# Kernel tuning notes

Measured on AMD Instinct MI355X. Metric: run time of the kernel, lower is better.

The kernel has to match this reference:

```python
import jax, jax.numpy as jnp
import numpy as np

EPS = 1e-5

def conv(x, w, b, stride, pad):
    y = jax.lax.conv_general_dilated(x, w, (stride, stride), [(pad, pad), (pad, pad)],
                                     dimension_numbers=('NCHW', 'OIHW', 'NCHW'))
    return y + b[None, :, None, None]

def inorm(x):
    # InstanceNorm2d, affine=False, eps=1e-5, biased variance over H,W
    m = x.mean(axis=(2, 3), keepdims=True)
    v = ((x - m) ** 2).mean(axis=(2, 3), keepdims=True)
    return (x - m) * jax.lax.rsqrt(v + EPS)

def setup_inputs() -> dict:
    key = jax.random.key(0)
    ks = jax.random.split(key, 24)
    B = 64
    x = jax.random.normal(ks[0], (B, 5, 256, 192), dtype=jnp.float32)
    chans = [(5, 8), (8, 16), (16, 32), (32, 64), (64, 128), (128, 256)]
    params = {'x': x}
    for i, (ci, co) in enumerate(chans):
        fan = ci * 16
        params[f'w{i}'] = jax.random.normal(ks[1 + 2 * i], (co, ci, 4, 4), jnp.float32) / np.sqrt(fan)
        params[f'b{i}'] = jnp.zeros((co,), jnp.float32)
    for i in (6, 7):
        params[f'w{i}'] = jax.random.normal(ks[1 + 2 * i], (256, 256, 3, 3), jnp.float32) / np.sqrt(256 * 9)
        params[f'b{i}'] = jnp.zeros((256,), jnp.float32)
    params['fc1_w'] = jax.random.normal(ks[20], (128, 512), jnp.float32) / np.sqrt(512)
    params['fc1_b'] = jnp.zeros((128,), jnp.float32)
    # fc2: weight zeroed at init in original; use small random for a nontrivial baseline
    params['fc2_w'] = jax.random.normal(ks[21], (50, 128), jnp.float32) * 0.01
    lin = np.linspace(-0.9, 0.9, 5, dtype=np.float32)
    yy, xx = np.meshgrid(lin, lin, indexing='ij')
    tcp = np.stack([xx.ravel(), yy.ravel()], axis=1)  # [25,2]
    params['fc2_b'] = jnp.asarray(np.arctanh(tcp).reshape(-1))  # [50]
    return params

def reference(x, w0, b0, w1, b1, w2, b2, w3, b3, w4, b4, w5, b5, w6, b6, w7, b7,
              fc1_w, fc1_b, fc2_w, fc2_b):
    B = x.shape[0]
    # block 0: conv -> relu -> instance_norm
    h = inorm(jax.nn.relu(conv(x, w0, b0, 2, 1)))
    # blocks 1..5: conv -> instance_norm -> relu, stride 2
    for w, b in ((w1, b1), (w2, b2), (w3, b3), (w4, b4), (w5, b5)):
        h = jax.nn.relu(inorm(conv(h, w, b, 2, 1)))
    # two 3x3 stride-1 blocks
    for w, b in ((w6, b6), (w7, b7)):
        h = jax.nn.relu(inorm(conv(h, w, b, 1, 1)))
    # maxpool 2x2 stride 2
    h = jax.lax.reduce_window(h, -jnp.inf, jax.lax.max, (1, 1, 2, 2), (1, 1, 2, 2), 'VALID')
    h = h.reshape(B, -1)  # [B,512]
    h = jax.nn.relu(h @ fc1_w.T + fc1_b)
    # F.dropout in eval mode = identity (reference is deterministic)
    pts = jnp.tanh(h @ fc2_w.T + fc2_b)  # [B,50]
    coor = pts.reshape(B, -1, 2)          # [B,25,2]
    grid = coor.reshape(B, 5, 5, 2)       # [B, row j, col i, (x,y)]

    # get_row: squared diffs along i, then abs second difference; stack order (j outer, i inner)
    d_row = (grid[:, :, 1:] - grid[:, :, :-1]) ** 2            # [B,5,4,2]
    row = jnp.abs(d_row[:, :, 1:] - d_row[:, :, :-1]).reshape(B, 15, 2)
    # get_col: same along j; stack order (i outer, j inner)
    gT = jnp.swapaxes(grid, 1, 2)                              # [B, i, j, 2]
    d_col = (gT[:, :, 1:] - gT[:, :, :-1]) ** 2
    col = jnp.abs(d_col[:, :, 1:] - d_col[:, :, :-1]).reshape(B, 15, 2)

    # grad_row / grad_col: curvature cross-product terms, BATCH ELEMENT 0 ONLY (as in original)
    def curv(g):  # g: [5,5,2], triplets along axis 1
        p0, p1, p2 = g[:, :-2], g[:, 1:-1], g[:, 2:]
        x0, y0 = p0[..., 0], p0[..., 1]
        x1, y1 = p1[..., 0], p1[..., 1]
        x2, y2 = p2[..., 0], p2[..., 1]
        return jnp.abs((y1 - y0) * (x1 - x2) - (y1 - y2) * (x1 - x0))  # [5,3]

    g0 = grid[0]
    rg_loss = jnp.maximum(curv(g0).sum(), 0.02)
    cg_loss = jnp.maximum(curv(jnp.swapaxes(g0, 0, 1)).sum(), 0.02)

    rx_loss = jnp.maximum(0.08, row[:, :, 0]).mean()
    ry_loss = jnp.maximum(0.08, row[:, :, 1]).mean()
    cx_loss = jnp.maximum(0.08, col[:, :, 0]).mean()
    cy_loss = jnp.maximum(0.08, col[:, :, 1]).mean()
    return (coor, rx_loss, ry_loss, cx_loss, cy_loss, rg_loss, cg_loss)
```

## Files before the change

### kernel.cpp

```cpp
#include <hip/hip_runtime.h>
#include <hip/hip_bf16.h>
#include <math.h>

#define EPS 1e-5f

template<int CIN, int COUT, int H, int W, int TPB>
__global__ __launch_bounds__(TPB) void conv42V(const float* __restrict__ in,
                                               const float* __restrict__ w,
                                               const float* __restrict__ bias,
                                               float* __restrict__ out, int relu)
{
    constexpr int OH  = H / 2, OW = W / 2;
    constexpr int NPX = OH * OW;
    constexpr int PXB = (NPX / 2) / TPB;
    constexpr int NCG = COUT / 8;

    __shared__ float sW[CIN * 8 * 16];
    __shared__ float sB[8];

    int t   = threadIdx.x;
    int bx  = blockIdx.x;
    int pxb = bx % PXB;
    int cg  = (bx / PXB) % NCG;
    int n   = bx / (PXB * NCG);
// ... 135 lines not shown

__global__ __launch_bounds__(256) void inorm_wave_T768(const float* __restrict__ src,
                                                       float* __restrict__ dst_t)
{
    int gid  = blockIdx.x * blockDim.x + threadIdx.x;
    int wv   = gid >> 6;
    int lane = gid & 63;
    int n = wv >> 5;
    int c = wv & 31;
    const float* p = src + (size_t)wv * 768;
    float tv[12];
    float s1 = 0.f, s2 = 0.f;
#pragma unroll
    for (int k = 0; k < 12; ++k) {
        float v = p[lane + k * 64];
        tv[k] = v;
        s1 += v; s2 += v * v;
    }
    for (int m = 32; m >= 1; m >>= 1) {
        s1 += __shfl_xor(s1, m);
        s2 += __shfl_xor(s2, m);
    }
    float mean = s1 * (1.f / 768.f);
    float var  = s2 * (1.f / 768.f) - mean * mean;
    float r = rsqrtf(var + EPS);
#pragma unroll
    for (int k = 0; k < 12; ++k) {
        int i = lane + k * 64;
        float y = fmaxf((tv[k] - mean) * r, 0.f);
        dst_t[((size_t)c * 768 + i) * 64 + n] = y;
    }
}

__global__ __launch_bounds__(256) void conv_l3t(const float* __restrict__ in_t,
                                                const float* __restrict__ w,
                                                float* __restrict__ pbuf)
{
    int t    = threadIdx.x;
    int lane = t & 63;
    int gw   = __builtin_amdgcn_readfirstlane(blockIdx.x * 4 + (t >> 6));
    int cog  = gw & 31;
    int cic  = (gw >> 5) & 3;
    int oh   = gw >> 7;
    int cc   = cic * 8;
    int co0  = cog * 2;
    int ih0  = 2 * oh - 1;

    float acc[2][12];
#pragma unroll
    for (int j = 0; j < 2; ++j)
#pragma unroll
        for (int p = 0; p < 12; ++p) acc[j][p] = 0.f;

    const float* wb = w + ((size_t)co0 * 32 + cc) * 16;

#pragma unroll 1
    for (int ci = 0; ci < 8; ++ci) {
        const float* pl = in_t + (size_t)(cc + ci) * 768 * 64 + lane;
        float wr[2][16];
#pragma unroll
        for (int k = 0; k < 16; ++k) {
            wr[0][k] = wb[(0 * 32 + ci) * 16 + k];
            wr[1][k] = wb[(1 * 32 + ci) * 16 + k];
        }
#pragma unroll
        for (int kh = 0; kh < 4; ++kh) {
            int ih = ih0 + kh;
            float p[26];
            p[0] = 0.f; p[25] = 0.f;
            if ((unsigned)ih < 32u) {
#pragma unroll
                for (int c = 0; c < 24; ++c)
                    p[c + 1] = pl[(size_t)(ih * 24 + c) * 64];
            } else {
#pragma unroll
                for (int c = 0; c < 24; ++c) p[c + 1] = 0.f;
            }
#pragma unroll
            for (int ow = 0; ow < 12; ++ow) {
#pragma unroll
                for (int kw = 0; kw < 4; ++kw) {
                    float pv = p[2 * ow + kw];
                    acc[0][ow] = fmaf(pv, wr[0][kh * 4 + kw], acc[0][ow]);
                    acc[1][ow] = fmaf(pv, wr[1][kh * 4 + kw], acc[1][ow]);
                }
            }
        }
    }

    float* pb = pbuf + ((size_t)cic * 4096 + (size_t)lane * 64 + co0) * 192 + oh * 12;
#pragma unroll
    for (int j = 0; j < 2; ++j) {
        float4* o4 = (float4*)(pb + (size_t)j * 192);
        o4[0] = make_float4(acc[j][0], acc[j][1], acc[j][2],  acc[j][3]);
        o4[1] = make_float4(acc[j][4], acc[j][5], acc[j][6],  acc[j][7]);
        o4[2] = make_float4(acc[j][8], acc[j][9], acc[j][10], acc[j][11]);
    }
}

__global__ __launch_bounds__(256) void reduce_norm_l3T(const float* __restrict__ pbuf,
                                                       float* __restrict__ dst_t)
{
    int gid  = blockIdx.x * blockDim.x + threadIdx.x;
    int wv   = gid >> 6;
    int lane = gid & 63;
    int n  = wv >> 6;
    int co = wv & 63;
    float tv[3];
#pragma unroll
    for (int k = 0; k < 3; ++k) {
        int i = lane + k * 64;
        float sum = 0.f;
#pragma unroll
        for (int s = 0; s < 4; ++s)
            sum += pbuf[((size_t)s * 4096 + wv) * 192 + i];
        tv[k] = sum;
    }
    float s1 = tv[0] + tv[1] + tv[2];
    float s2 = tv[0]*tv[0] + tv[1]*tv[1] + tv[2]*tv[2];
    for (int m = 32; m >= 1; m >>= 1) {
        s1 += __shfl_xor(s1, m);
        s2 += __shfl_xor(s2, m);
    }
    float mean = s1 * (1.f / 192.f);
    float var  = s2 * (1.f / 192.f) - mean * mean;
    float r = rsqrtf(var + EPS);
#pragma unroll
    for (int k = 0; k < 3; ++k) {
        int i = lane + k * 64;
        float y = fmaxf((tv[k] - mean) * r, 0.f);
        dst_t[((size_t)co * 192 + i) * 64 + n] = y;
    }
}

template<int TPB, int VPT>
__global__ void inorm_blockv(float* __restrict__ data, int relu)
{
    const int HW = TPB * VPT * 4;
    float4* p = (float4*)(data + (size_t)blockIdx.x * HW);
    float4 v[VPT];
    float s = 0.f, q = 0.f;
#pragma unroll
    for (int k = 0; k < VPT; ++k) {
        v[k] = p[threadIdx.x + k * TPB];
        s += v[k].x + v[k].y + v[k].z + v[k].w;
        q += v[k].x*v[k].x + v[k].y*v[k].y + v[k].z*v[k].z + v[k].w*v[k].w;
    }
    for (int m2 = 32; m2 >= 1; m2 >>= 1) {
        s += __shfl_xor(s, m2);
        q += __shfl_xor(q, m2);
    }
    __shared__ float ss[TPB / 64], sq[TPB / 64], sm[2];
    int wave = threadIdx.x >> 6, lane = threadIdx.x & 63;
    if (lane == 0) { ss[wave] = s; sq[wave] = q; }
    __syncthreads();
    if (threadIdx.x == 0) {
        float a = 0.f, b2 = 0.f;
#pragma unroll
        for (int k = 0; k < TPB / 64; ++k) { a += ss[k]; b2 += sq[k]; }
        float mm = a / (float)HW;
        float vv = b2 / (float)HW - mm * mm;
        sm[0] = mm; sm[1] = rsqrtf(vv + EPS);
    }
    __syncthreads();
    float m = sm[0], r = sm[1];
#pragma unroll
    for (int k = 0; k < VPT; ++k) {
        float4 y;
        y.x = (v[k].x - m) * r; y.y = (v[k].y - m) * r;
        y.z = (v[k].z - m) * r; y.w = (v[k].w - m) * r;
        if (relu) {
            y.x = fmaxf(y.x, 0.f); y.y = fmaxf(y.y, 0.f);
            y.z = fmaxf(y.z, 0.f); y.w = fmaxf(y.w, 0.f);
        }
        p[threadIdx.x + k * TPB] = y;
    }
}

__global__ __launch_bounds__(256) void conv_l4(const float* __restrict__ in_t,
                                               const float* __restrict__ w,
                                               float* __restrict__ pbuf)
{
    int t    = threadIdx.x;
    int lane = t & 63;
    int gw   = __builtin_amdgcn_readfirstlane(blockIdx.x * 4 + (t >> 6));
    int cog  = gw & 63;
    int cic  = (gw >> 6) & 7;
    int half = gw >> 9;
    int cc   = cic * 8;
    int co0  = cog * 2;
    int oh0  = half * 4;

    float acc[2][24];
#pragma unroll
    for (int j = 0; j < 2; ++j)
#pragma unroll
        for (int p = 0; p < 24; ++p) acc[j][p] = 0.f;

    const float* wp = w + ((size_t)co0 * 64 + cc) * 16;

#pragma unroll 1
    for (int ci = 0; ci < 8; ++ci) {
        const float* pl = in_t + (size_t)(cc + ci) * 192 * 64 + lane;
        float wr[2][16];
#pragma unroll
        for (int k = 0; k < 16; ++k) {
            wr[0][k] = wp[(0 * 64 + ci) * 16 + k];
            wr[1][k] = wp[(1 * 64 + ci) * 16 + k];
        }
#pragma unroll
        for (int kh = 0; kh < 4; ++kh) {
            float p[4][12];
#pragma unroll
            for (int o = 0; o < 4; ++o) {
                int ih = 2 * (oh0 + o) - 1 + kh;
                if ((unsigned)ih < 16u) {
#pragma unroll
                    for (int c = 0; c < 12; ++c)
                        p[o][c] = pl[(size_t)(ih * 12 + c) * 64];
                } else {
#pragma unroll
                    for (int c = 0; c < 12; ++c) p[o][c] = 0.f;
                }
            }
#pragma unroll
            for (int o = 0; o < 4; ++o)
#pragma unroll
                for (int ow = 0; ow < 6; ++ow) {
#pragma unroll
                    for (int kw = 0; kw < 4; ++kw) {
                        int iw = 2 * ow - 1 + kw;
                        if (iw < 0 || iw >= 12) continue;
                        float pv = p[o][iw];
                        acc[0][o * 6 + ow] = fmaf(pv, wr[0][kh * 4 + kw], acc[0][o * 6 + ow]);
                        acc[1][o * 6 + ow] = fmaf(pv, wr[1][kh * 4 + kw], acc[1][o * 6 + ow]);
                    }
                }
        }
    }

    float* pb = pbuf + ((size_t)(cic * 64 + lane) * 128 + co0) * 48 + oh0 * 6;
#pragma unroll
    for (int j = 0; j < 2; ++j) {
        float4* o4 = (float4*)(pb + j * 48);
#pragma unroll
        for (int q = 0; q < 6; ++q)
            o4[q] = make_float4(acc[j][q * 4 + 0], acc[j][q * 4 + 1],
                                acc[j][q * 4 + 2], acc[j][q * 4 + 3]);
    }
}

__global__ __launch_bounds__(256) void reduce_norm48(const float* __restrict__ pbuf,
                                                     float* __restrict__ out)
{
    int g  = blockIdx.x * blockDim.x + threadIdx.x;
    int co = g & 127;
    int n  = g >> 7;
    float s[48];
#pragma unroll
    for (int p = 0; p < 48; ++p) s[p] = 0.f;
#pragma unroll 1
    for (int c = 0; c < 8; ++c) {
        const float4* p4 = (const float4*)(pbuf + ((size_t)(c * 64 + n) * 128 + co) * 48);
#pragma unroll
        for (int q = 0; q < 12; ++q) {
            float4 a = p4[q];
            s[q * 4 + 0] += a.x; s[q * 4 + 1] += a.y;
            s[q * 4 + 2] += a.z; s[q * 4 + 3] += a.w;
        }
    }
    float m = 0.f;
#pragma unroll
    for (int p = 0; p < 48; ++p) m += s[p];
    m *= (1.f / 48.f);
    float q = 0.f;
#pragma unroll
    for (int p = 0; p < 48; ++p) { float d = s[p] - m; q += d * d; }
    q *= (1.f / 48.f);
    float r = rsqrtf(q + EPS);
    float4* o4 = (float4*)(out + ((size_t)n * 128 + co) * 48);
#pragma unroll
    for (int qq = 0; qq < 12; ++qq) {
        float4 v;
        v.x = fmaxf((s[qq * 4 + 0] - m) * r, 0.f);
        v.y = fmaxf((s[qq * 4 + 1] - m) * r, 0.f);
        v.z = fmaxf((s[qq * 4 + 2] - m) * r, 0.f);
        v.w = fmaxf((s[qq * 4 + 3] - m) * r, 0.f);
        o4[qq] = v;
    }
}

__global__ __launch_bounds__(256) void conv_l67(const float* __restrict__ in,
                                                const float* __restrict__ w,
                                                float* __restrict__ pbuf)
{
    int t    = threadIdx.x;
    int gw   = __builtin_amdgcn_readfirstlane(blockIdx.x * 4 + (t >> 6));
    int lane = t & 63;
    int cic  = gw >> 6;
    int cog  = gw & 63;
    int cc   = cic * 16;
    int co0  = cog * 4;

    float acc[4][12];
#pragma unroll
    for (int j = 0; j < 4; ++j)
#pragma unroll
        for (int p = 0; p < 12; ++p) acc[j][p] = 0.f;

    const float* ip = in + ((size_t)lane * 256 + cc) * 12;
    const float* wp = w + ((size_t)co0 * 256 + cc) * 9;

#pragma unroll 2
    for (int ci = 0; ci < 16; ++ci) {
        float p[12];
        const float4* p4 = (const float4*)(ip + ci * 12);
        float4 a0 = p4[0], a1 = p4[1], a2 = p4[2];
        p[0] = a0.x; p[1] = a0.y; p[2]  = a0.z; p[3]  = a0.w;
        p[4] = a1.x; p[5] = a1.y; p[6]  = a1.z; p[7]  = a1.w;
        p[8] = a2.x; p[9] = a2.y; p[10] = a2.z; p[11] = a2.w;
#pragma unroll
        for (int j = 0; j < 4; ++j) {
            const float* wj = wp + ((size_t)j * 256 + ci) * 9;
            float wr[9];
#pragma unroll
            for (int k = 0; k < 9; ++k) wr[k] = wj[k];
#pragma unroll
            for (int oh = 0; oh < 4; ++oh)
#pragma unroll
                for (int ow = 0; ow < 3; ++ow)
#pragma unroll
                    for (int kh = 0; kh < 3; ++kh) {
                        int ih = oh - 1 + kh;
                        if (ih < 0 || ih >= 4) continue;
#pragma unroll
                        for (int kw = 0; kw < 3; ++kw) {
                            int iw = ow - 1 + kw;
                            if (iw < 0 || iw >= 3) continue;
                            acc[j][oh * 3 + ow] =
                                fmaf(p[ih * 3 + iw], wr[kh * 3 + kw], acc[j][oh * 3 + ow]);
                        }
                    }
        }
    }

    float* pb = pbuf + ((size_t)(cic * 64 + lane) * 256 + co0) * 12;
#pragma unroll
    for (int j = 0; j < 4; ++j) {
        float4* o4 = (float4*)(pb + j * 12);
        o4[0] = make_float4(acc[j][0], acc[j][1], acc[j][2],  acc[j][3]);
        o4[1] = make_float4(acc[j][4], acc[j][5], acc[j][6],  acc[j][7]);
        o4[2] = make_float4(acc[j][8], acc[j][9], acc[j][10], acc[j][11]);
    }
}

__global__ __launch_bounds__(256) void conv_l5(const float* __restrict__ in,
                                               const float* __restrict__ w,
                                               float* __restrict__ pbuf)
{
    int t    = threadIdx.x;
    int gw   = __builtin_amdgcn_readfirstlane(blockIdx.x * 4 + (t >> 6));
    int lane = t & 63;
    int cic  = gw >> 6;
    int cog  = gw & 63;
    int cc   = cic * 8;
    int co0  = cog * 4;

    float acc[4][12];
#pragma unroll
    for (int j = 0; j < 4; ++j)
#pragma unroll
        for (int p = 0; p < 12; ++p) acc[j][p] = 0.f;

    const float* ip = in + ((size_t)lane * 128 + cc) * 48;
    const float* wp = w + ((size_t)co0 * 128 + cc) * 16;

#pragma unroll 1
    for (int ci = 0; ci < 8; ++ci) {
        float p[48];
        const float4* p4 = (const float4*)(ip + ci * 48);
#pragma unroll
        for (int q = 0; q < 12; ++q) {
            float4 a = p4[q];
            p[q * 4 + 0] = a.x; p[q * 4 + 1] = a.y; p[q * 4 + 2] = a.z; p[q * 4 + 3] = a.w;
        }
#pragma unroll
        for (int j = 0; j < 4; ++j) {
            const float* wj = wp + ((size_t)j * 128 + ci) * 16;
            float wr[16];
#pragma unroll
            for (int k = 0; k < 16; ++k) wr[k] = wj[k];
#pragma unroll
            for (int oh = 0; oh < 4; ++oh)
#pragma unroll
                for (int ow = 0; ow < 3; ++ow) {
                    int ih0 = 2 * oh - 1, iw0 = 2 * ow - 1;
#pragma unroll
                    for (int kh = 0; kh < 4; ++kh) {
                        int ih = ih0 + kh;
                        if (ih < 0 || ih >= 8) continue;
#pragma unroll
                        for (int kw = 0; kw < 4; ++kw) {
                            int iw = iw0 + kw;
                            if (iw < 0 || iw >= 6) continue;
                            acc[j][oh * 3 + ow] =
                                fmaf(p[ih * 6 + iw], wr[kh * 4 + kw], acc[j][oh * 3 + ow]);
                        }
                    }
                }
        }
    }

    float* pb = pbuf + ((size_t)(cic * 64 + lane) * 256 + co0) * 12;
#pragma unroll
    for (int j = 0; j < 4; ++j) {
        float4* o4 = (float4*)(pb + j * 12);
        o4[0] = make_float4(acc[j][0], acc[j][1], acc[j][2],  acc[j][3]);
        o4[1] = make_float4(acc[j][4], acc[j][5], acc[j][6],  acc[j][7]);
        o4[2] = make_float4(acc[j][8], acc[j][9], acc[j][10], acc[j][11]);
    }
}

__global__ __launch_bounds__(256) void reduce_norm12(const float* __restrict__ pbuf,
                                                     float* __restrict__ out)
{
    int g  = blockIdx.x * blockDim.x + threadIdx.x;
    int co = g & 255;
    int n  = g >> 8;
    float s[12];
#pragma unroll
    for (int p = 0; p < 12; ++p) s[p] = 0.f;
#pragma unroll 1
    for (int c = 0; c < 16; ++c) {
        const float4* p4 = (const float4*)(pbuf + ((size_t)(c * 64 + n) * 256 + co) * 12);
        float4 a = p4[0], b = p4[1], d = p4[2];
        s[0] += a.x; s[1] += a.y; s[2]  += a.z; s[3]  += a.w;
        s[4] += b.x; s[5] += b.y; s[6]  += b.z; s[7]  += b.w;
        s[8] += d.x; s[9] += d.y; s[10] += d.z; s[11] += d.w;
    }
    float m = 0.f;
#pragma unroll
    for (int p = 0; p < 12; ++p) m += s[p];
    m *= (1.f / 12.f);
    float q = 0.f;
#pragma unroll
    for (int p = 0; p < 12; ++p) { float d = s[p] - m; q += d * d; }
    q *= (1.f / 12.f);
    float r = rsqrtf(q + EPS);
    float* op = out + ((size_t)n * 256 + co) * 12;
    float4* o4 = (float4*)op;
    float y[12];
#pragma unroll
    for (int p = 0; p < 12; ++p) y[p] = fmaxf((s[p] - m) * r, 0.f);
    o4[0] = make_float4(y[0], y[1], y[2],  y[3]);
    o4[1] = make_float4(y[4], y[5], y[6],  y[7]);
    o4[2] = make_float4(y[8], y[9], y[10], y[11]);
}

__global__ void pool_kernel(const float* __restrict__ in, float* __restrict__ out)
{
    int idx = blockIdx.x * blockDim.x + threadIdx.x;
    if (idx >= 64 * 512) return;
    int f = idx & 511;
    int n = idx >> 9;
    int c = f >> 1;
    int h = f & 1;
    const float* p = in + (((size_t)n * 256 + c) * 4 + h * 2) * 3;
    out[idx] = fmaxf(fmaxf(p[0], p[1]), fmaxf(p[3], p[4]));
}

__global__ void fc1_kernel(const float* __restrict__ in, const float* __restrict__ w,
                           const float* __restrict__ b, float* __restrict__ out)
{
    int idx = blockIdx.x * blockDim.x + threadIdx.x;
    if (idx >= 64 * 128) return;
    int j = idx & 127;
    int n = idx >> 7;
    const float* x  = in + n * 512;
    const float* wr = w + j * 512;
    float acc = b[j];
    for (int f = 0; f < 512; ++f) acc = fmaf(x[f], wr[f], acc);
    out[idx] = fmaxf(acc, 0.f);
}

__global__ void fc2_kernel(const float* __restrict__ in, const float* __restrict__ w,
                           const float* __restrict__ b, float* __restrict__ out)
{
    int idx = blockIdx.x * blockDim.x + threadIdx.x;
    if (idx >= 64 * 50) return;
    int k = idx % 50;
    int n = idx / 50;
    const float* x  = in + n * 128;
    const float* wr = w + k * 128;
    float acc = b[k];
    for (int f = 0; f < 128; ++f) acc = fmaf(x[f], wr[f], acc);
    out[idx] = tanhf(acc);
}

__global__ void loss_kernel(const float* __restrict__ pts, float* __restrict__ out)
{
    __shared__ float acc[4][64];
    int n = threadIdx.x;
    float rx = 0.f, ry = 0.f, cx = 0.f, cy = 0.f;
    {
        const float* g = pts + n * 50;
        for (int r = 0; r < 5; ++r)
            for (int j = 0; j < 3; ++j)
                for (int d = 0; d < 2; ++d) {
                    float a0 = g[(r * 5 + j) * 2 + d];
                    float a1 = g[(r * 5 + j + 1) * 2 + d];
                    float a2 = g[(r * 5 + j + 2) * 2 + d];
                    float d0 = (a1 - a0) * (a1 - a0);
                    float d1 = (a2 - a1) * (a2 - a1);
                    float t = fmaxf(0.08f, fabsf(d1 - d0));
                    if (d == 0) rx += t; else ry += t;
                }
        for (int r = 0; r < 5; ++r)
            for (int j = 0; j < 3; ++j)
                for (int d = 0; d < 2; ++d) {
                    float a0 = g[(j * 5 + r) * 2 + d];
                    float a1 = g[((j + 1) * 5 + r) * 2 + d];
                    float a2 = g[((j + 2) * 5 + r) * 2 + d];
                    float d0 = (a1 - a0) * (a1 - a0);
                    float d1 = (a2 - a1) * (a2 - a1);
                    float t = fmaxf(0.08f, fabsf(d1 - d0));
                    if (d == 0) cx += t; else cy += t;
                }
    }
    acc[0][n] = rx; acc[1][n] = ry; acc[2][n] = cx; acc[3][n] = cy;
    __syncthreads();
    if (n == 0) {
        float s0 = 0.f, s1 = 0.f, s2 = 0.f, s3 = 0.f;
        for (int i = 0; i < 64; ++i) {
            s0 += acc[0][i]; s1 += acc[1][i]; s2 += acc[2][i]; s3 += acc[3][i];
        }
        float inv = 1.0f / (64.0f * 15.0f);
        out[3200] = s0 * inv;
        out[3201] = s1 * inv;
        out[3202] = s2 * inv;
        out[3203] = s3 * inv;
        const float* g = pts;
        float rg = 0.f, cg = 0.f;
        for (int r = 0; r < 5; ++r)
            for (int j = 0; j < 3; ++j) {
                float x0 = g[(r * 5 + j) * 2],     y0 = g[(r * 5 + j) * 2 + 1];
                float x1 = g[(r * 5 + j + 1) * 2], y1 = g[(r * 5 + j + 1) * 2 + 1];
                float x2 = g[(r * 5 + j + 2) * 2], y2 = g[(r * 5 + j + 2) * 2 + 1];
                rg += fabsf((y1 - y0) * (x1 - x2) - (y1 - y2) * (x1 - x0));
            }
        for (int r = 0; r < 5; ++r)
            for (int j = 0; j < 3; ++j) {
                float x0 = g[(j * 5 + r) * 2],       y0 = g[(j * 5 + r) * 2 + 1];
                float x1 = g[((j + 1) * 5 + r) * 2], y1 = g[((j + 1) * 5 + r) * 2 + 1];
                float x2 = g[((j + 2) * 5 + r) * 2], y2 = g[((j + 2) * 5 + r) * 2 + 1];
                cg += fabsf((y1 - y0) * (x1 - x2) - (y1 - y2) * (x1 - x0));
            }
        out[3204] = fmaxf(rg, 0.02f);
        out[3205] = fmaxf(cg, 0.02f);
    }
}

extern "C" void kernel_launch(void* const* d_in, const int* in_sizes, int n_in,
                              void* d_out, int out_size, void* d_ws, size_t ws_size,
                              hipStream_t stream)
{
    const float* x = (const float*)d_in[0];
    const float* w[8], *bia[8];
    for (int i = 0; i < 6; ++i) { w[i] = (const float*)d_in[1 + 2 * i]; bia[i] = (const float*)d_in[2 + 2 * i]; }
    w[6] = (const float*)d_in[13]; bia[6] = (const float*)d_in[14];
    w[7] = (const float*)d_in[15]; bia[7] = (const float*)d_in[16];
    const float* fc1_w = (const float*)d_in[17];
    const float* fc1_b = (const float*)d_in[18];
    const float* fc2_w = (const float*)d_in[19];
    const float* fc2_b = (const float*)d_in[20];
    float* out = (float*)d_out;

    float* A      = (float*)d_ws;
    float* Bf     = A + 6291456;
    float* pooled = Bf + 3145728;
    float* fc1o   = pooled + 32768;
    float* At2    = A + 1572864;
    float* pbuf3  = A + 3145728;
    float* At     = A;
    float* l4out  = A + 1048576;
    float* pbuf   = A + 3145728;

    const int N = 64;

    conv0<<<1536, 256, 0, stream>>>(x, w[0], bia[0], A);
    inorm_blockv<256, 12><<<N * 8, 256, 0, stream>>>(A, 0);

    conv42V<8, 16, 128, 96, 256><<<768, 256, 0, stream>>>(A, w[1], bia[1], Bf, 0);
    inorm_blockv<256, 3><<<N * 16, 256, 0, stream>>>(Bf, 1);

    conv42V<16, 32, 64, 48, 192><<<512, 192, 0, stream>>>(Bf, w[2], bia[2], A, 0);
    inorm_wave_T768<<<512, 256, 0, stream>>>(A, At2);

    conv_l3t<<<512, 256, 0, stream>>>(At2, w[3], pbuf3);
    reduce_norm_l3T<<<1024, 256, 0, stream>>>(pbuf3, At);

    conv_l4<<<256, 256, 0, stream>>>(At, w[4], pbuf);
    reduce_norm48<<<32, 256, 0, stream>>>(pbuf, l4out);

    conv_l5<<<256, 256, 0, stream>>>(l4out, w[5], pbuf);
    reduce_norm12<<<64, 256, 0, stream>>>(pbuf, Bf);

    conv_l67<<<256, 256, 0, stream>>>(Bf, w[6], pbuf);
    reduce_norm12<<<64, 256, 0, stream>>>(pbuf, A);

    conv_l67<<<256, 256, 0, stream>>>(A, w[7], pbuf);
    float* l7out = Bf + 262144;
    reduce_norm12<<<64, 256, 0, stream>>>(pbuf, l7out);

    pool_kernel<<<(64 * 512 + 255) / 256, 256, 0, stream>>>(l7out, pooled);
    fc1_kernel<<<(64 * 128 + 255) / 256, 256, 0, stream>>>(pooled, fc1_w, fc1_b, fc1o);
    fc2_kernel<<<(64 * 50 + 255) / 256, 256, 0, stream>>>(fc1o, fc2_w, fc2_b, out);
    loss_kernel<<<1, 64, 0, stream>>>(out, out);
}
```

Measured before the change: 423.3 us.

## Fuse conv with instance-norm reduction for layers 4-7 and merge tail kernels

Layers 4 to 7 now run one kernel per layer. Each block owns one output channel and reduces partial sums across input-channel splits in shared memory, then applies instance norm and ReLU in the same kernel. This removes the global partial-sum buffer and the separate reduce kernels. Pool plus fc1, and fc2 plus the loss, are each merged into one kernel to cut launch count. The cost is less parallelism: 128 or 256 blocks each doing longer serial input-channel loops, and fc2 plus the loss run in a single block.

After: 591.0 us. +39.6%, slower.

```diff
diff --git a/kernel.cpp b/kernel.cpp
--- a/kernel.cpp
+++ b/kernel.cpp
@@ -191,107 +191,6 @@
     }
 }
 
-__global__ __launch_bounds__(256) void conv_l3t(const float* __restrict__ in_t,
-                                                const float* __restrict__ w,
-                                                float* __restrict__ pbuf)
-{
-    int t    = threadIdx.x;
-    int lane = t & 63;
-    int gw   = __builtin_amdgcn_readfirstlane(blockIdx.x * 4 + (t >> 6));
-    int cog  = gw & 31;
-    int cic  = (gw >> 5) & 3;
-    int oh   = gw >> 7;
-    int cc   = cic * 8;
-    int co0  = cog * 2;
-    int ih0  = 2 * oh - 1;
-
-    float acc[2][12];
-#pragma unroll
-    for (int j = 0; j < 2; ++j)
-#pragma unroll
-        for (int p = 0; p < 12; ++p) acc[j][p] = 0.f;
-
-    const float* wb = w + ((size_t)co0 * 32 + cc) * 16;
-
-#pragma unroll 1
-    for (int ci = 0; ci < 8; ++ci) {
-        const float* pl = in_t + (size_t)(cc + ci) * 768 * 64 + lane;
-        float wr[2][16];
-#pragma unroll
-        for (int k = 0; k < 16; ++k) {
-            wr[0][k] = wb[(0 * 32 + ci) * 16 + k];
-            wr[1][k] = wb[(1 * 32 + ci) * 16 + k];
-        }
-#pragma unroll
-        for (int kh = 0; kh < 4; ++kh) {
-            int ih = ih0 + kh;
-            float p[26];
-            p[0] = 0.f; p[25] = 0.f;
-            if ((unsigned)ih < 32u) {
-#pragma unroll
-                for (int c = 0; c < 24; ++c)
-                    p[c + 1] = pl[(size_t)(ih * 24 + c) * 64];
-            } else {
-#pragma unroll
-                for (int c = 0; c < 24; ++c) p[c + 1] = 0.f;
-            }
-#pragma unroll
-            for (int ow = 0; ow < 12; ++ow) {
-#pragma unroll
-                for (int kw = 0; kw < 4; ++kw) {
-                    float pv = p[2 * ow + kw];
-                    acc[0][ow] = fmaf(pv, wr[0][kh * 4 + kw], acc[0][ow]);
-                    acc[1][ow] = fmaf(pv, wr[1][kh * 4 + kw], acc[1][ow]);
-                }
-            }
-        }
-    }
-
-    float* pb = pbuf + ((size_t)cic * 4096 + (size_t)lane * 64 + co0) * 192 + oh * 12;
-#pragma unroll
-    for (int j = 0; j < 2; ++j) {
-        float4* o4 = (float4*)(pb + (size_t)j * 192);
-        o4[0] = make_float4(acc[j][0], acc[j][1], acc[j][2],  acc[j][3]);
-        o4[1] = make_float4(acc[j][4], acc[j][5], acc[j][6],  acc[j][7]);
-        o4[2] = make_float4(acc[j][8], acc[j][9], acc[j][10], acc[j][11]);
-    }
-}
-
-__global__ __launch_bounds__(256) void reduce_norm_l3T(const float* __restrict__ pbuf,
-                                                       float* __restrict__ dst_t)
-{
-    int gid  = blockIdx.x * blockDim.x + threadIdx.x;
-    int wv   = gid >> 6;
-    int lane = gid & 63;
-    int n  = wv >> 6;
-    int co = wv & 63;
-    float tv[3];
-#pragma unroll
-    for (int k = 0; k < 3; ++k) {
-        int i = lane + k * 64;
-        float sum = 0.f;
-#pragma unroll
-        for (int s = 0; s < 4; ++s)
-            sum += pbuf[((size_t)s * 4096 + wv) * 192 + i];
-        tv[k] = sum;
-    }
-    float s1 = tv[0] + tv[1] + tv[2];
-    float s2 = tv[0]*tv[0] + tv[1]*tv[1] + tv[2]*tv[2];
-    for (int m = 32; m >= 1; m >>= 1) {
-        s1 += __shfl_xor(s1, m);
-        s2 += __shfl_xor(s2, m);
-    }
-    float mean = s1 * (1.f / 192.f);
-    float var  = s2 * (1.f / 192.f) - mean * mean;
-    float r = rsqrtf(var + EPS);
-#pragma unroll
-    for (int k = 0; k < 3; ++k) {
-        int i = lane + k * 64;
-        float y = fmaxf((tv[k] - mean) * r, 0.f);
-        dst_t[((size_t)co * 192 + i) * 64 + n] = y;
-    }
-}
-
 template<int TPB, int VPT>
 __global__ void inorm_blockv(float* __restrict__ data, int relu)
 {
@@ -336,37 +235,129 @@
     }
 }
 
-__global__ __launch_bounds__(256) void conv_l4(const float* __restrict__ in_t,
-                                               const float* __restrict__ w,
-                                               float* __restrict__ pbuf)
+__global__ __launch_bounds__(256) void k_l3conv(const float* __restrict__ At2,
+                                                const float* __restrict__ w3,
+                                                float* __restrict__ pbuf)
 {
     int t    = threadIdx.x;
     int lane = t & 63;
-    int gw   = __builtin_amdgcn_readfirstlane(blockIdx.x * 4 + (t >> 6));
-    int cog  = gw & 63;
-    int cic  = (gw >> 6) & 7;
-    int half = gw >> 9;
-    int cc   = cic * 8;
-    int co0  = cog * 2;
-    int oh0  = half * 4;
-
-    float acc[2][24];
+    int wid  = __builtin_amdgcn_readfirstlane(blockIdx.x * 4 + (t >> 6));
+    int cog = wid & 31;
+    int cic = (wid >> 5) & 3;
+    int oh  = wid >> 7;
+    int cc  = cic * 8;
+    int co0 = cog * 2;
+    int ih0 = 2 * oh - 1;
+
+    float acc[2][12];
 #pragma unroll
     for (int j = 0; j < 2; ++j)
 #pragma unroll
-        for (int p = 0; p < 24; ++p) acc[j][p] = 0.f;
-
-    const float* wp = w + ((size_t)co0 * 64 + cc) * 16;
+        for (int p = 0; p < 12; ++p) acc[j][p] = 0.f;
+
+    const float* wb = w3 + ((size_t)co0 * 32 + cc) * 16;
 
 #pragma unroll 1
     for (int ci = 0; ci < 8; ++ci) {
-        const float* pl = in_t + (size_t)(cc + ci) * 192 * 64 + lane;
+        const float* pl = At2 + (size_t)(cc + ci) * 768 * 64 + lane;
         float wr[2][16];
 #pragma unroll
         for (int k = 0; k < 16; ++k) {
-            wr[0][k] = wp[(0 * 64 + ci) * 16 + k];
-            wr[1][k] = wp[(1 * 64 + ci) * 16 + k];
-        }
+            wr[0][k] = wb[(0 * 32 + ci) * 16 + k];
+            wr[1][k] = wb[(1 * 32 + ci) * 16 + k];
+        }
+#pragma unroll
+        for (int kh = 0; kh < 4; ++kh) {
+            int ih = ih0 + kh;
+            float p[26];
+            p[0] = 0.f; p[25] = 0.f;
+            if ((unsigned)ih < 32u) {
+#pragma unroll
+                for (int c = 0; c < 24; ++c)
+                    p[c + 1] = pl[(size_t)(ih * 24 + c) * 64];
+            } else {
+#pragma unroll
+                for (int c = 0; c < 24; ++c) p[c + 1] = 0.f;
+            }
+#pragma unroll
+            for (int ow = 0; ow < 12; ++ow) {
+#pragma unroll
+                for (int kw = 0; kw < 4; ++kw) {
+                    float pv = p[2 * ow + kw];
+                    acc[0][ow] = fmaf(pv, wr[0][kh * 4 + kw], acc[0][ow]);
+                    acc[1][ow] = fmaf(pv, wr[1][kh * 4 + kw], acc[1][ow]);
+                }
+            }
+        }
+    }
+    float* pb = pbuf + ((size_t)cic * 4096 + (size_t)lane * 64 + co0) * 192 + oh * 12;
+#pragma unroll
+    for (int j = 0; j < 2; ++j) {
+        float4* o4 = (float4*)(pb + (size_t)j * 192);
+        o4[0] = make_float4(acc[j][0], acc[j][1], acc[j][2],  acc[j][3]);
+        o4[1] = make_float4(acc[j][4], acc[j][5], acc[j][6],  acc[j][7]);
+        o4[2] = make_float4(acc[j][8], acc[j][9], acc[j][10], acc[j][11]);
+    }
+}
+
+__global__ __launch_bounds__(256) void k_l3red(const float* __restrict__ pbuf,
+                                               float* __restrict__ At)
+{
+    int gid  = blockIdx.x * blockDim.x + threadIdx.x;
+    int wv   = gid >> 6;
+    int lane = gid & 63;
+    int n  = wv >> 6;
+    int co = wv & 63;
+    float tv[3];
+#pragma unroll
+    for (int k = 0; k < 3; ++k) {
+        int i = lane + k * 64;
+        float sum = 0.f;
+#pragma unroll
+        for (int s = 0; s < 4; ++s)
+            sum += pbuf[((size_t)s * 4096 + wv) * 192 + i];
+        tv[k] = sum;
+    }
+    float s1 = tv[0] + tv[1] + tv[2];
+    float s2 = tv[0]*tv[0] + tv[1]*tv[1] + tv[2]*tv[2];
+    for (int m = 32; m >= 1; m >>= 1) {
+        s1 += __shfl_xor(s1, m);
+        s2 += __shfl_xor(s2, m);
+    }
+    float mean = s1 * (1.f / 192.f);
+    float var  = s2 * (1.f / 192.f) - mean * mean;
+    float r = rsqrtf(var + EPS);
+#pragma unroll
+    for (int k = 0; k < 3; ++k) {
+        int i = lane + k * 64;
+        float y = fmaxf((tv[k] - mean) * r, 0.f);
+        At[((size_t)co * 192 + i) * 64 + n] = y;
+    }
+}
+
+__global__ __launch_bounds__(256) void l4_fused(const float* __restrict__ At,
+                                                const float* __restrict__ w4,
+                                                float* __restrict__ out)
+{
+    __shared__ float part[2][2][64][24];
+    __shared__ float ex[2][64][2];
+    int t = threadIdx.x, lane = t & 63, w = t >> 6;
+    int half = w >> 1, cic = w & 1;
+    int co = blockIdx.x;
+    int oh0 = half * 4;
+
+    float acc[24];
+#pragma unroll
+    for (int p = 0; p < 24; ++p) acc[p] = 0.f;
+
+    const float* wp = w4 + ((size_t)co * 64 + cic * 32) * 16;
+
+#pragma unroll 1
+    for (int ci = 0; ci < 32; ++ci) {
+        const float* pl = At + (size_t)(cic * 32 + ci) * 192 * 64 + lane;
+        float wr[16];
+#pragma unroll
+        for (int k = 0; k < 16; ++k) wr[k] = wp[ci * 16 + k];
 #pragma unroll
         for (int kh = 0; kh < 4; ++kh) {
             float p[4][12];
@@ -390,332 +381,282 @@
                     for (int kw = 0; kw < 4; ++kw) {
                         int iw = 2 * ow - 1 + kw;
                         if (iw < 0 || iw >= 12) continue;
-                        float pv = p[o][iw];
-                        acc[0][o * 6 + ow] = fmaf(pv, wr[0][kh * 4 + kw], acc[0][o * 6 + ow]);
-                        acc[1][o * 6 + ow] = fmaf(pv, wr[1][kh * 4 + kw], acc[1][o * 6 + ow]);
+                        acc[o * 6 + ow] = fmaf(p[o][iw], wr[kh * 4 + kw], acc[o * 6 + ow]);
                     }
                 }
         }
     }
-
-    float* pb = pbuf + ((size_t)(cic * 64 + lane) * 128 + co0) * 48 + oh0 * 6;
-#pragma unroll
-    for (int j = 0; j < 2; ++j) {
-        float4* o4 = (float4*)(pb + j * 48);
-#pragma unroll
-        for (int q = 0; q < 6; ++q)
-            o4[q] = make_float4(acc[j][q * 4 + 0], acc[j][q * 4 + 1],
-                                acc[j][q * 4 + 2], acc[j][q * 4 + 3]);
-    }
-}
-
-__global__ __launch_bounds__(256) void reduce_norm48(const float* __restrict__ pbuf,
-                                                     float* __restrict__ out)
-{
-    int g  = blockIdx.x * blockDim.x + threadIdx.x;
-    int co = g & 127;
-    int n  = g >> 7;
-    float s[48];
-#pragma unroll
-    for (int p = 0; p < 48; ++p) s[p] = 0.f;
+#pragma unroll
+    for (int p = 0; p < 24; ++p) part[half][cic][lane][p] = acc[p];
+    __syncthreads();
+
+    int h = w & 1;
+    float s[24];
+    float s1 = 0.f, s2 = 0.f;
+#pragma unroll
+    for (int p = 0; p < 24; ++p) {
+        s[p] = part[h][0][lane][p] + part[h][1][lane][p];
+        s1 += s[p]; s2 += s[p] * s[p];
+    }
+    if (w < 2) { ex[h][lane][0] = s1; ex[h][lane][1] = s2; }
+    __syncthreads();
+    float S1 = ex[0][lane][0] + ex[1][lane][0];
+    float S2 = ex[0][lane][1] + ex[1][lane][1];
+    float mean = S1 * (1.f / 48.f);
+    float var  = S2 * (1.f / 48.f) - mean * mean;
+    float r = rsqrtf(var + EPS);
+    if (w < 2) {
+        float4* o4 = (float4*)(out + ((size_t)lane * 128 + co) * 48 + h * 24);
+#pragma unroll
+        for (int q = 0; q < 6; ++q) {
+            float4 v;
+            v.x = fmaxf((s[q * 4 + 0] - mean) * r, 0.f);
+            v.y = fmaxf((s[q * 4 + 1] - mean) * r, 0.f);
+            v.z = fmaxf((s[q * 4 + 2] - mean) * r, 0.f);
+            v.w = fmaxf((s[q * 4 + 3] - mean) * r, 0.f);
+            o4[q] = v;
+        }
+    }
+}
+
+__global__ __launch_bounds__(256) void l5_fused(const float* __restrict__ in,
+                                                const float* __restrict__ w5,
+                                                float* __restrict__ out)
+{
+    __shared__ float part[4][64][12];
+    int t = threadIdx.x, lane = t & 63, w = t >> 6;
+    int co = blockIdx.x;
+
+    float acc[12];
+#pragma unroll
+    for (int p = 0; p < 12; ++p) acc[p] = 0.f;
+
+    const float* ip = in + ((size_t)lane * 128 + w * 32) * 48;
+    const float* wp = w5 + ((size_t)co * 128 + w * 32) * 16;
+
 #pragma unroll 1
-    for (int c = 0; c < 8; ++c) {
-        const float4* p4 = (const float4*)(pbuf + ((size_t)(c * 64 + n) * 128 + co) * 48);
+    for (int ci = 0; ci < 32; ++ci) {
+        float p[48];
+        const float4* p4 = (const float4*)(ip + ci * 48);
 #pragma unroll
         for (int q = 0; q < 12; ++q) {
             float4 a = p4[q];
-            s[q * 4 + 0] += a.x; s[q * 4 + 1] += a.y;
-            s[q * 4 + 2] += a.z; s[q * 4 + 3] += a.w;
-        }
-    }
-    float m = 0.f;
-#pragma unroll
-    for (int p = 0; p < 48; ++p) m += s[p];
-    m *= (1.f / 48.f);
-    float q = 0.f;
-#pragma unroll
-    for (int p = 0; p < 48; ++p) { float d = s[p] - m; q += d * d; }
-    q *= (1.f / 48.f);
-    float r = rsqrtf(q + EPS);
-    float4* o4 = (float4*)(out + ((size_t)n * 128 + co) * 48);
-#pragma unroll
-    for (int qq = 0; qq < 12; ++qq) {
-        float4 v;
-        v.x = fmaxf((s[qq * 4 + 0] - m) * r, 0.f);
-        v.y = fmaxf((s[qq * 4 + 1] - m) * r, 0.f);
-        v.z = fmaxf((s[qq * 4 + 2] - m) * r, 0.f);
-        v.w = fmaxf((s[qq * 4 + 3] - m) * r, 0.f);
-        o4[qq] = v;
-    }
-}
-
-__global__ __launch_bounds__(256) void conv_l67(const float* __restrict__ in,
-                                                const float* __restrict__ w,
-                                                float* __restrict__ pbuf)
-{
-    int t    = threadIdx.x;
-    int gw   = __builtin_amdgcn_readfirstlane(blockIdx.x * 4 + (t >> 6));
-    int lane = t & 63;
-    int cic  = gw >> 6;
-    int cog  = gw & 63;
-    int cc   = cic * 16;
-    int co0  = cog * 4;
-
-    float acc[4][12];
-#pragma unroll
-    for (int j = 0; j < 4; ++j)
-#pragma unroll
-        for (int p = 0; p < 12; ++p) acc[j][p] = 0.f;
-
-    const float* ip = in + ((size_t)lane * 256 + cc) * 12;
-    const float* wp = w + ((size_t)co0 * 256 + cc) * 9;
+            p[q * 4 + 0] = a.x; p[q * 4 + 1] = a.y;
+            p[q * 4 + 2] = a.z; p[q * 4 + 3] = a.w;
+        }
+        float wr[16];
+#pragma unroll
+        for (int k = 0; k < 16; ++k) wr[k] = wp[ci * 16 + k];
+#pragma unroll
+        for (int oh = 0; oh < 4; ++oh)
+#pragma unroll
+            for (int ow = 0; ow < 3; ++ow) {
+                int ih0 = 2 * oh - 1, iw0 = 2 * ow - 1;
+#pragma unroll
+                for (int kh = 0; kh < 4; ++kh) {
+                    int ih = ih0 + kh;
+                    if (ih < 0 || ih >= 8) continue;
+#pragma unroll
+                    for (int kw = 0; kw < 4; ++kw) {
+                        int iw = iw0 + kw;
+                        if (iw < 0 || iw >= 6) continue;
+                        acc[oh * 3 + ow] = fmaf(p[ih * 6 + iw], wr[kh * 4 + kw], acc[oh * 3 + ow]);
+                    }
+                }
+            }
+    }
+#pragma unroll
+    for (int p = 0; p < 12; ++p) part[w][lane][p] = acc[p];
+    __syncthreads();
+    if (w == 0) {
+        float s[12];
+        float s1 = 0.f, s2 = 0.f;
+#pragma unroll
+        for (int p = 0; p < 12; ++p) {
+            s[p] = part[0][lane][p] + part[1][lane][p] + part[2][lane][p] + part[3][lane][p];
+            s1 += s[p]; s2 += s[p] * s[p];
+        }
+        float mean = s1 * (1.f / 12.f);
+        float var  = s2 * (1.f / 12.f) - mean * mean;
+        float r = rsqrtf(var + EPS);
+        float y[12];
+#pragma unroll
+        for (int p = 0; p < 12; ++p) y[p] = fmaxf((s[p] - mean) * r, 0.f);
+        float4* o4 = (float4*)(out + ((size_t)lane * 256 + co) * 12);
+        o4[0] = make_float4(y[0], y[1], y[2],  y[3]);
+        o4[1] = make_float4(y[4], y[5], y[6],  y[7]);
+        o4[2] = make_float4(y[8], y[9], y[10], y[11]);
+    }
+}
+
+__global__ __launch_bounds__(256) void l67_fused(const float* __restrict__ in,
+                                                 const float* __restrict__ wgt,
+                                                 float* __restrict__ out)
+{
+    __shared__ float part[4][64][12];
+    int t = threadIdx.x, lane = t & 63, w = t >> 6;
+    int co = blockIdx.x;
+
+    float acc[12];
+#pragma unroll
+    for (int p = 0; p < 12; ++p) acc[p] = 0.f;
+
+    const float* ip = in + ((size_t)lane * 256 + w * 64) * 12;
+    const float* wp = wgt + ((size_t)co * 256 + w * 64) * 9;
 
 #pragma unroll 2
-    for (int ci = 0; ci < 16; ++ci) {
+    for (int ci = 0; ci < 64; ++ci) {
         float p[12];
         const float4* p4 = (const float4*)(ip + ci * 12);
         float4 a0 = p4[0], a1 = p4[1], a2 = p4[2];
         p[0] = a0.x; p[1] = a0.y; p[2]  = a0.z; p[3]  = a0.w;
         p[4] = a1.x; p[5] = a1.y; p[6]  = a1.z; p[7]  = a1.w;
         p[8] = a2.x; p[9] = a2.y; p[10] = a2.z; p[11] = a2.w;
-#pragma unroll
-        for (int j = 0; j < 4; ++j) {
-            const float* wj = wp + ((size_t)j * 256 + ci) * 9;
-            float wr[9];
-#pragma unroll
-            for (int k = 0; k < 9; ++k) wr[k] = wj[k];
-#pragma unroll
-            for (int oh = 0; oh < 4; ++oh)
-#pragma unroll
-                for (int ow = 0; ow < 3; ++ow)
-#pragma unroll
-                    for (int kh = 0; kh < 3; ++kh) {
-                        int ih = oh - 1 + kh;
-                        if (ih < 0 || ih >= 4) continue;
-#pragma unroll
-                        for (int kw = 0; kw < 3; ++kw) {
-                            int iw = ow - 1 + kw;
-                            if (iw < 0 || iw >= 3) continue;
-                            acc[j][oh * 3 + ow] =
-                                fmaf(p[ih * 3 + iw], wr[kh * 3 + kw], acc[j][oh * 3 + ow]);
-                        }
-                    }
-        }
-    }
-
-    float* pb = pbuf + ((size_t)(cic * 64 + lane) * 256 + co0) * 12;
-#pragma unroll
-    for (int j = 0; j < 4; ++j) {
-        float4* o4 = (float4*)(pb + j * 12);
-        o4[0] = make_float4(acc[j][0], acc[j][1], acc[j][2],  acc[j][3]);
-        o4[1] = make_float4(acc[j][4], acc[j][5], acc[j][6],  acc[j][7]);
-        o4[2] = make_float4(acc[j][8], acc[j][9], acc[j][10], acc[j][11]);
-    }
-}
-
-__global__ __launch_bounds__(256) void conv_l5(const float* __restrict__ in,
-                                               const float* __restrict__ w,
-                                               float* __restrict__ pbuf)
-{
-    int t    = threadIdx.x;
-    int gw   = __builtin_amdgcn_readfirstlane(blockIdx.x * 4 + (t >> 6));
-    int lane = t & 63;
-    int cic  = gw >> 6;
-    int cog  = gw & 63;
-    int cc   = cic * 8;
-    int co0  = cog * 4;
-
-    float acc[4][12];
-#pragma unroll
-    for (int j = 0; j < 4; ++j)
-#pragma unroll
-        for (int p = 0; p < 12; ++p) acc[j][p] = 0.f;
-
-    const float* ip = in + ((size_t)lane * 128 + cc) * 48;
-    const float* wp = w + ((size_t)co0 * 128 + cc) * 16;
-
-#pragma unroll 1
-    for (int ci = 0; ci < 8; ++ci) {
-        float p[48];
-        const float4* p4 = (const float4*)(ip + ci * 48);
-#pragma unroll
-        for (int q = 0; q < 12; ++q) {
-            float4 a = p4[q];
-            p[q * 4 + 0] = a.x; p[q * 4 + 1] = a.y; p[q * 4 + 2] = a.z; p[q * 4 + 3] = a.w;
-        }
-#pragma unroll
-        for (int j = 0; j < 4; ++j) {
-            const float* wj = wp + ((size_t)j * 128 + ci) * 16;
-            float wr[16];
-#pragma unroll
-            for (int k = 0; k < 16; ++k) wr[k] = wj[k];
-#pragma unroll
-            for (int oh = 0; oh < 4; ++oh)
-#pragma unroll
-                for (int ow = 0; ow < 3; ++ow) {
-                    int ih0 = 2 * oh - 1, iw0 = 2 * ow - 1;
-#pragma unroll
-                    for (int kh = 0; kh < 4; ++kh) {
-                        int ih = ih0 + kh;
-                        if (ih < 0 || ih >= 8) continue;
-#pragma unroll
-                        for (int kw = 0; kw < 4; ++kw) {
-                            int iw = iw0 + kw;
-                            if (iw < 0 || iw >= 6) continue;
-                            acc[j][oh * 3 + ow] =
-                                fmaf(p[ih * 6 + iw], wr[kh * 4 + kw], acc[j][oh * 3 + ow]);
-                        }
+        float wr[9];
+#pragma unroll
+        for (int k = 0; k < 9; ++k) wr[k] = wp[ci * 9 + k];
+#pragma unroll
+        for (int oh = 0; oh < 4; ++oh)
+#pragma unroll
+            for (int ow = 0; ow < 3; ++ow)
+#pragma unroll
+                for (int kh = 0; kh < 3; ++kh) {
+                    int ih = oh - 1 + kh;
+                    if (ih < 0 || ih >= 4) continue;
+#pragma unroll
+                    for (int kw = 0; kw < 3; ++kw) {
+                        int iw = ow - 1 + kw;
+                        if (iw < 0 || iw >= 3) continue;
+                        acc[oh * 3 + ow] = fmaf(p[ih * 3 + iw], wr[kh * 3 + kw], acc[oh * 3 + ow]);
                     }
                 }
-        }
-    }
-
-    float* pb = pbuf + ((size_t)(cic * 64 + lane) * 256 + co0) * 12;
-#pragma unroll
-    for (int j = 0; j < 4; ++j) {
-        float4* o4 = (float4*)(pb + j * 12);
-        o4[0] = make_float4(acc[j][0], acc[j][1], acc[j][2],  acc[j][3]);
-        o4[1] = make_float4(acc[j][4], acc[j][5], acc[j][6],  acc[j][7]);
-        o4[2] = make_float4(acc[j][8], acc[j][9], acc[j][10], acc[j][11]);
-    }
-}
-
-__global__ __launch_bounds__(256) void reduce_norm12(const float* __restrict__ pbuf,
-                                                     float* __restrict__ out)
-{
-    int g  = blockIdx.x * blockDim.x + threadIdx.x;
-    int co = g & 255;
-    int n  = g >> 8;
-    float s[12];
-#pragma unroll
-    for (int p = 0; p < 12; ++p) s[p] = 0.f;
-#pragma unroll 1
-    for (int c = 0; c < 16; ++c) {
-        const float4* p4 = (const float4*)(pbuf + ((size_t)(c * 64 + n) * 256 + co) * 12);
-        float4 a = p4[0], b = p4[1], d = p4[2];
-        s[0] += a.x; s[1] += a.y; s[2]  += a.z; s[3]  += a.w;
-        s[4] += b.x; s[5] += b.y; s[6]  += b.z; s[7]  += b.w;
-        s[8] += d.x; s[9] += d.y; s[10] += d.z; s[11] += d.w;
-    }
-    float m = 0.f;
-#pragma unroll
-    for (int p = 0; p < 12; ++p) m += s[p];
-    m *= (1.f / 12.f);
-    float q = 0.f;
-#pragma unroll
-    for (int p = 0; p < 12; ++p) { float d = s[p] - m; q += d * d; }
-    q *= (1.f / 12.f);
-    float r = rsqrtf(q + EPS);
-    float* op = out + ((size_t)n * 256 + co) * 12;
-    float4* o4 = (float4*)op;
-    float y[12];
-#pragma unroll
-    for (int p = 0; p < 12; ++p) y[p] = fmaxf((s[p] - m) * r, 0.f);
-    o4[0] = make_float4(y[0], y[1], y[2],  y[3]);
-    o4[1] = make_float4(y[4], y[5], y[6],  y[7]);
-    o4[2] = make_float4(y[8], y[9], y[10], y[11]);
-}
-
-__global__ void pool_kernel(const float* __restrict__ in, float* __restrict__ out)
-{
-    int idx = blockIdx.x * blockDim.x + threadIdx.x;
-    if (idx >= 64 * 512) return;
-    int f = idx & 511;
-    int n = idx >> 9;
-    int c = f >> 1;
-    int h = f & 1;
-    const float* p = in + (((size_t)n * 256 + c) * 4 + h * 2) * 3;
-    out[idx] = fmaxf(fmaxf(p[0], p[1]), fmaxf(p[3], p[4]));
-}
-
-__global__ void fc1_kernel(const float* __restrict__ in, const float* __restrict__ w,
-                           const float* __restrict__ b, float* __restrict__ out)
-{
-    int idx = blockIdx.x * blockDim.x + threadIdx.x;
-    if (idx >= 64 * 128) return;
-    int j = idx & 127;
-    int n = idx >> 7;
-    const float* x  = in + n * 512;
-    const float* wr = w + j * 512;
-    float acc = b[j];
-    for (int f = 0; f < 512; ++f) acc = fmaf(x[f], wr[f], acc);
-    out[idx] = fmaxf(acc, 0.f);
-}
-
-__global__ void fc2_kernel(const float* __restrict__ in, const float* __restrict__ w,
-                           const float* __restrict__ b, float* __restrict__ out)
-{
-    int idx = blockIdx.x * blockDim.x + threadIdx.x;
-    if (idx >= 64 * 50) return;
-    int k = idx % 50;
-    int n = idx / 50;
-    const float* x  = in + n * 128;
-    const float* wr = w + k * 128;
-    float acc = b[k];
-    for (int f = 0; f < 128; ++f) acc = fmaf(x[f], wr[f], acc);
-    out[idx] = tanhf(acc);
-}
-
-__global__ void loss_kernel(const float* __restrict__ pts, float* __restrict__ out)
-{
-    __shared__ float acc[4][64];
-    int n = threadIdx.x;
-    float rx = 0.f, ry = 0.f, cx = 0.f, cy = 0.f;
-    {
-        const float* g = pts + n * 50;
+    }
+#pragma unroll
+    for (int p = 0; p < 12; ++p) part[w][lane][p] = acc[p];
+    __syncthreads();
+    if (w == 0) {
+        float s[12];
+        float s1 = 0.f, s2 = 0.f;
+#pragma unroll
+        for (int p = 0; p < 12; ++p) {
+            s[p] = part[0][lane][p] + part[1][lane][p] + part[2][lane][p] + part[3][lane][p];
+            s1 += s[p]; s2 += s[p] * s[p];
+        }
+        float mean = s1 * (1.f / 12.f);
+        float var  = s2 * (1.f / 12.f) - mean * mean;
+        float r = rsqrtf(var + EPS);
+        float y[12];
+#pragma unroll
+        for (int p = 0; p < 12; ++p) y[p] = fmaxf((s[p] - mean) * r, 0.f);
+        float4* o4 = (float4*)(out + ((size_t)lane * 256 + co) * 12);
+        o4[0] = make_float4(y[0], y[1], y[2],  y[3]);
+        o4[1] = make_float4(y[4], y[5], y[6],  y[7]);
+        o4[2] = make_float4(y[8], y[9], y[10], y[11]);
+    }
+}
+
+__global__ __launch_bounds__(128) void pool_fc1(const float* __restrict__ in,
+                                                const float* __restrict__ fc1_w,
+                                                const float* __restrict__ fc1_b,
+                                                float* __restrict__ fc1o)
+{
+    __shared__ float sPool[512];
+    int t = threadIdx.x;
+    int n = blockIdx.x;
+    for (int f = t; f < 512; f += 128) {
+        int c = f >> 1;
+        int h = f & 1;
+        const float* p = in + (((size_t)n * 256 + c) * 4 + h * 2) * 3;
+        sPool[f] = fmaxf(fmaxf(p[0], p[1]), fmaxf(p[3], p[4]));
+    }
+    __syncthreads();
+    const float* wr = fc1_w + t * 512;
+    float acc = fc1_b[t];
+#pragma unroll 4
+    for (int f = 0; f < 512; ++f) acc = fmaf(sPool[f], wr[f], acc);
+    fc1o[n * 128 + t] = fmaxf(acc, 0.f);
+}
+
+__global__ __launch_bounds__(256) void fc2_loss(const float* __restrict__ fc1o,
+                                                const float* __restrict__ fc2_w,
+                                                const float* __restrict__ fc2_b,
+                                                float* __restrict__ out)
+{
+    __shared__ float sPts[3200];
+    __shared__ float sAcc[4 * 64];
+    int t = threadIdx.x;
+    for (int idx = t; idx < 3200; idx += 256) {
+        int n = idx / 50;
+        int k = idx % 50;
+        const float* xv = fc1o + n * 128;
+        const float* wr = fc2_w + k * 128;
+        float acc = fc2_b[k];
+#pragma unroll 4
+        for (int f = 0; f < 128; ++f) acc = fmaf(xv[f], wr[f], acc);
+        float v = tanhf(acc);
+        out[idx]  = v;
+        sPts[idx] = v;
+    }
+    __syncthreads();
+    if (t < 64) {
+        int n = t;
+        float rx = 0.f, ry = 0.f, cx = 0.f, cy = 0.f;
+        const float* gp = sPts + n * 50;
         for (int r = 0; r < 5; ++r)
             for (int j = 0; j < 3; ++j)
                 for (int d = 0; d < 2; ++d) {
-                    float a0 = g[(r * 5 + j) * 2 + d];
-                    float a1 = g[(r * 5 + j + 1) * 2 + d];
-                    float a2 = g[(r * 5 + j + 2) * 2 + d];
+                    float a0 = gp[(r * 5 + j) * 2 + d];
+                    float a1 = gp[(r * 5 + j + 1) * 2 + d];
+                    float a2 = gp[(r * 5 + j + 2) * 2 + d];
                     float d0 = (a1 - a0) * (a1 - a0);
                     float d1 = (a2 - a1) * (a2 - a1);
-                    float t = fmaxf(0.08f, fabsf(d1 - d0));
-                    if (d == 0) rx += t; else ry += t;
+                    float tt = fmaxf(0.08f, fabsf(d1 - d0));
+                    if (d == 0) rx += tt; else ry += tt;
                 }
         for (int r = 0; r < 5; ++r)
             for (int j = 0; j < 3; ++j)
                 for (int d = 0; d < 2; ++d) {
-                    float a0 = g[(j * 5 + r) * 2 + d];
-                    float a1 = g[((j + 1) * 5 + r) * 2 + d];
-                    float a2 = g[((j + 2) * 5 + r) * 2 + d];
+                    float a0 = gp[(j * 5 + r) * 2 + d];
+                    float a1 = gp[((j + 1) * 5 + r) * 2 + d];
+                    float a2 = gp[((j + 2) * 5 + r) * 2 + d];
                     float d0 = (a1 - a0) * (a1 - a0);
                     float d1 = (a2 - a1) * (a2 - a1);
-                    float t = fmaxf(0.08f, fabsf(d1 - d0));
-                    if (d == 0) cx += t; else cy += t;
+                    float tt = fmaxf(0.08f, fabsf(d1 - d0));
+                    if (d == 0) cx += tt; else cy += tt;
                 }
-    }
-    acc[0][n] = rx; acc[1][n] = ry; acc[2][n] = cx; acc[3][n] = cy;
-    __syncthreads();
-    if (n == 0) {
+        sAcc[0 * 64 + n] = rx; sAcc[1 * 64 + n] = ry;
+        sAcc[2 * 64 + n] = cx; sAcc[3 * 64 + n] = cy;
+    }
+    __syncthreads();
+    if (t == 0) {
         float s0 = 0.f, s1 = 0.f, s2 = 0.f, s3 = 0.f;
         for (int i = 0; i < 64; ++i) {
-            s0 += acc[0][i]; s1 += acc[1][i]; s2 += acc[2][i]; s3 += acc[3][i];
+            s0 += sAcc[0 * 64 + i]; s1 += sAcc[1 * 64 + i];
+            s2 += sAcc[2 * 64 + i]; s3 += sAcc[3 * 64 + i];
         }
         float inv = 1.0f / (64.0f * 15.0f);
         out[3200] = s0 * inv;
         out[3201] = s1 * inv;
         out[3202] = s2 * inv;
         out[3203] = s3 * inv;
-        const float* g = pts;
-        float rg = 0.f, cg = 0.f;
+        const float* gp = sPts;
+        float rg = 0.f, cgs = 0.f;
         for (int r = 0; r < 5; ++r)
             for (int j = 0; j < 3; ++j) {
-                float x0 = g[(r * 5 + j) * 2],     y0 = g[(r * 5 + j) * 2 + 1];
-                float x1 = g[(r * 5 + j + 1) * 2], y1 = g[(r * 5 + j + 1) * 2 + 1];
-                float x2 = g[(r * 5 + j + 2) * 2], y2 = g[(r * 5 + j + 2) * 2 + 1];
+                float x0 = gp[(r * 5 + j) * 2],     y0 = gp[(r * 5 + j) * 2 + 1];
+                float x1 = gp[(r * 5 + j + 1) * 2], y1 = gp[(r * 5 + j + 1) * 2 + 1];
+                float x2 = gp[(r * 5 + j + 2) * 2], y2 = gp[(r * 5 + j + 2) * 2 + 1];
                 rg += fabsf((y1 - y0) * (x1 - x2) - (y1 - y2) * (x1 - x0));
             }
         for (int r = 0; r < 5; ++r)
             for (int j = 0; j < 3; ++j) {
-                float x0 = g[(j * 5 + r) * 2],       y0 = g[(j * 5 + r) * 2 + 1];
-                float x1 = g[((j + 1) * 5 + r) * 2], y1 = g[((j + 1) * 5 + r) * 2 + 1];
-                float x2 = g[((j + 2) * 5 + r) * 2], y2 = g[((j + 2) * 5 + r) * 2 + 1];
-                cg += fabsf((y1 - y0) * (x1 - x2) - (y1 - y2) * (x1 - x0));
+                float x0 = gp[(j * 5 + r) * 2],       y0 = gp[(j * 5 + r) * 2 + 1];
+                float x1 = gp[((j + 1) * 5 + r) * 2], y1 = gp[((j + 1) * 5 + r) * 2 + 1];
+                float x2 = gp[((j + 2) * 5 + r) * 2], y2 = gp[((j + 2) * 5 + r) * 2 + 1];
+                cgs += fabsf((y1 - y0) * (x1 - x2) - (y1 - y2) * (x1 - x0));
             }
         out[3204] = fmaxf(rg, 0.02f);
-        out[3205] = fmaxf(cg, 0.02f);
+        out[3205] = fmaxf(cgs, 0.02f);
     }
 }
 
@@ -734,15 +675,14 @@
     const float* fc2_b = (const float*)d_in[20];
     float* out = (float*)d_out;
 
-    float* A      = (float*)d_ws;
-    float* Bf     = A + 6291456;
-    float* pooled = Bf + 3145728;
-    float* fc1o   = pooled + 32768;
-    float* At2    = A + 1572864;
-    float* pbuf3  = A + 3145728;
-    float* At     = A;
-    float* l4out  = A + 1048576;
-    float* pbuf   = A + 3145728;
+    float* A     = (float*)d_ws;
+    float* Bf    = A + 6291456;
+    float* At    = A;
+    float* At2   = A + 1572864;
+    float* l4out = A + 1048576;
+    float* pbuf  = A + 3145728;
+    float* fc1o  = A + 2097152;
+    float* l7out = Bf + 262144;
 
     const int N = 64;
 
@@ -755,24 +695,14 @@
     conv42V<16, 32, 64, 48, 192><<<512, 192, 0, stream>>>(Bf, w[2], bia[2], A, 0);
     inorm_wave_T768<<<512, 256, 0, stream>>>(A, At2);
 
-    conv_l3t<<<512, 256, 0, stream>>>(At2, w[3], pbuf3);
-    reduce_norm_l3T<<<1024, 256, 0, stream>>>(pbuf3, At);
-
-    conv_l4<<<256, 256, 0, stream>>>(At, w[4], pbuf);
-    reduce_norm48<<<32, 256, 0, stream>>>(pbuf, l4out);
-
-    conv_l5<<<256, 256, 0, stream>>>(l4out, w[5], pbuf);
-    reduce_norm12<<<64, 256, 0, stream>>>(pbuf, Bf);
-
-    conv_l67<<<256, 256, 0, stream>>>(Bf, w[6], pbuf);
-    reduce_norm12<<<64, 256, 0, stream>>>(pbuf, A);
-
-    conv_l67<<<256, 256, 0, stream>>>(A, w[7], pbuf);
-    float* l7out = Bf + 262144;
-    reduce_norm12<<<64, 256, 0, stream>>>(pbuf, l7out);
-
-    pool_kernel<<<(64 * 512 + 255) / 256, 256, 0, stream>>>(l7out, pooled);
-    fc1_kernel<<<(64 * 128 + 255) / 256, 256, 0, stream>>>(pooled, fc1_w, fc1_b, fc1o);
-    fc2_kernel<<<(64 * 50 + 255) / 256, 256, 0, stream>>>(fc1o, fc2_w, fc2_b, out);
-    loss_kernel<<<1, 64, 0, stream>>>(out, out);
-}
+    k_l3conv<<<512, 256, 0, stream>>>(At2, w[3], pbuf);
+    k_l3red<<<1024, 256, 0, stream>>>(pbuf, At);
+
+    l4_fused<<<128, 256, 0, stream>>>(At, w[4], l4out);
+    l5_fused<<<256, 256, 0, stream>>>(l4out, w[5], Bf);
+    l67_fused<<<256, 256, 0, stream>>>(Bf, w[6], A);
+    l67_fused<<<256, 256, 0, stream>>>(A, w[7], l7out);
+
+    pool_fc1<<<64, 128, 0, stream>>>(l7out, fc1_w, fc1_b, fc1o);
+    fc2_loss<<<1, 256, 0, stream>>>(fc1o, fc2_w, fc2_b, out);
+}
```
